# Optimization experiments

Hardware: AMD Instinct MI355X
Metric: run time of the kernel (lower is better)

Reference implementation:

```python
import jax, jax.numpy as jnp
import numpy as np

B, T, C, HS = 8, 2048, 1024, 64


def setup_inputs() -> dict:
    key = jax.random.key(0)
    ks = jax.random.split(key, 4)
    x = jax.random.normal(ks[0], (B, T, C), dtype=jnp.float32)
    Wq = jax.random.normal(ks[1], (C, HS), dtype=jnp.float32) * (C ** -0.5)
    Wk = jax.random.normal(ks[2], (C, HS), dtype=jnp.float32) * (C ** -0.5)
    Wv = jax.random.normal(ks[3], (C, HS), dtype=jnp.float32) * (C ** -0.5)
    mask = jnp.tril(jnp.ones((T, T), dtype=jnp.int32))  # causal mask
    return {"x": x, "mask": mask, "Wq": Wq, "Wk": Wk, "Wv": Wv}


def reference(x, mask, Wq, Wk, Wv):
    # x: [B,T,C]; bias-free projections to head_size
    q = jnp.einsum("btc,ch->bth", x, Wq)
    k = jnp.einsum("btc,ch->bth", x, Wk)
    v = jnp.einsum("btc,ch->bth", x, Wv)
    # NOTE: original scales by C**-0.5 (n_embd), not head_size**-0.5
    wei = jnp.einsum("bth,bsh->bts", q, k) * (x.shape[-1] ** -0.5)
    wei = jnp.where(mask[None, :, :] == 0, -jnp.inf, wei)
    wei = jax.nn.softmax(wei, axis=-1)
    # dropout is identity in eval / p=0
    out = jnp.einsum("bts,bsh->bth", wei, v)
    return out
```

## Files before the change

### kernel.cpp

```cpp
#include <hip/hip_runtime.h>
#include <hip/hip_bf16.h>


#define B_  8
#define T_  2048
#define C_  1024
#define HS_ 64
#define MROWS (B_ * T_)

typedef __attribute__((ext_vector_type(8))) short bf16x8;
typedef __attribute__((ext_vector_type(4))) float f32x4;
typedef __attribute__((ext_vector_type(4))) float float4v;

#define SCALE_LOG2 0.04508422037445829f

__device__ __forceinline__ short f2bs(float f) {
    __hip_bfloat16 h = __float2bfloat16(f);
    short s;
    __builtin_memcpy(&s, &h, 2);
    return s;
}

__global__ __launch_bounds__(256) void wt_kernel(
    const float* __restrict__ Wq,
    const float* __restrict__ Wk,
    const float* __restrict__ Wv,
    __hip_bfloat16* __restrict__ Wt) {
    __shared__ float tile[64][65];
    const int m  = blockIdx.x >> 4;
    const int r0 = (blockIdx.x & 15) * 64;
    const float* W = (m == 0) ? Wq : (m == 1) ? Wk : Wv;
    const int i = threadIdx.x >> 6;
    const int j = threadIdx.x & 63;
#pragma unroll
    for (int p = 0; p < 16; ++p) {
        int r = p * 4 + i;
        tile[r][j] = W[(size_t)(r0 + r) * HS_ + j];
    }
    __syncthreads();
#pragma unroll
    for (int p = 0; p < 16; ++p) {
        int h = p * 4 + i;
        Wt[(size_t)m * (HS_ * C_) + (size_t)h * C_ + r0 + j] =
            __float2bfloat16(tile[j][h]);
    }
}

__global__ __launch_bounds__(256, 2) void proj_kernel(
    const float* __restrict__ x,
    const __hip_bfloat16* __restrict__ Wt,
    __hip_bfloat16* __restrict__ Q,
    __hip_bfloat16* __restrict__ Kp,
    __hip_bfloat16* __restrict__ Vt)
{
    __shared__ float xt0[32 * 68];
    __shared__ float xt1[32 * 68];

    const int lane = threadIdx.x & 63;
    const int wave = threadIdx.x >> 6;
    const int quad = lane >> 4;
    const int l15  = lane & 15;
    const int row0 = blockIdx.x * 32;

    const float* gsrc[8];
#pragma unroll
    for (int rr = 0; rr < 8; ++rr)
        gsrc[rr] = x + (size_t)(row0 + wave * 8 + rr) * C_ + lane;

    const __hip_bfloat16* wbase[3];
#pragma unroll
    for (int j = 0; j < 3; ++j) {
        int nt = wave * 3 + j;
        int h  = ((nt & 3) * 16) + l15;
        wbase[j] = Wt + (size_t)(nt >> 2) * (HS_ * C_) + (size_t)h * C_ + quad * 8;
    }

    f32x4 acc[2][3];
#pragma unroll
    for (int rt = 0; rt < 2; ++rt)
#pragma unroll
        for (int j = 0; j < 3; ++j)
            acc[rt][j] = (f32x4){0.f, 0.f, 0.f, 0.f};

    bf16x8 bfr0[2][3], bfr1[2][3];

#define ISSUE_DMA(XT, kc)                                                    \
    do {                                                                     \
        _Pragma("unroll")                                                    \
        for (int rr = 0; rr < 8; ++rr)                                       \
            __builtin_amdgcn_global_load_lds(                                \
                (const __attribute__((address_space(1))) unsigned*)          \
                    (gsrc[rr] + (kc)),                                       \
                (__attribute__((address_space(3))) unsigned*)                \
                    (&XT[(wave * 8 + rr) * 68]),                             \
                4, 0, 0);                                                    \
    } while (0)

#define LOAD_B(BF, kc)                                                       \
    do {                                                                     \
        _Pragma("unroll")                                                    \
        for (int ks = 0; ks < 2; ++ks)                                       \
            _Pragma("unroll")                                                \
            for (int j = 0; j < 3; ++j)                                      \
                BF[ks][j] = *(const bf16x8*)(wbase[j] + (kc) + ks * 32);     \
    } while (0)

#define COMPUTE(XT, BF)                                                      \
    do {                                                                     \
        _Pragma("unroll")                                                    \
        for (int ks = 0; ks < 2; ++ks) {                                     \
            bf16x8 a[2];                                                     \
            _Pragma("unroll")                                                \
            for (int rt = 0; rt < 2; ++rt) {                                 \
                const float4v* p = (const float4v*)                          \
                    &XT[(rt * 16 + l15) * 68 + ks * 32 + quad * 8];          \
                float4v f0 = p[0], f1 = p[1];                                \
                _Pragma("unroll")                                            \
                for (int e = 0; e < 4; ++e) {                                \
                    a[rt][e]     = f2bs(f0[e]);                              \
                    a[rt][4 + e] = f2bs(f1[e]);                              \
                }                                                            \
            }                                                                \
            _Pragma("unroll")                                                \
            for (int rt = 0; rt < 2; ++rt)                                   \
                _Pragma("unroll")                                            \
                for (int j = 0; j < 3; ++j)                                  \
                    acc[rt][j] = __builtin_amdgcn_mfma_f32_16x16x32_bf16(    \
                        a[rt], BF[ks][j], acc[rt][j], 0, 0, 0);              \
        }                                                                    \
    } while (0)

    ISSUE_DMA(xt0, 0);
    LOAD_B(bfr0, 0);

#pragma unroll 1
    for (int kc = 0; kc < C_; kc += 128) {
        __syncthreads();
        if (kc + 64 < C_) {
            ISSUE_DMA(xt1, kc + 64);
            LOAD_B(bfr1, kc + 64);
        }
        COMPUTE(xt0, bfr0);
        __syncthreads();
        if (kc + 128 < C_) {
            ISSUE_DMA(xt0, kc + 128);
            LOAD_B(bfr0, kc + 128);
        }
        COMPUTE(xt1, bfr1);
    }
#undef ISSUE_DMA
#undef LOAD_B
#undef COMPUTE

#pragma unroll
    for (int rt = 0; rt < 2; ++rt) {
#pragma unroll
        for (int j = 0; j < 3; ++j) {
            int nt  = wave * 3 + j;
            int mtx = nt >> 2;
            int col = (nt & 3) * 16 + l15;
#pragma unroll
            for (int r = 0; r < 4; ++r) {
                int row = row0 + rt * 16 + quad * 4 + r;
                __hip_bfloat16 v = __float2bfloat16(acc[rt][j][r]);
                if (mtx == 0) {
                    Q[(size_t)row * HS_ + col] = v;
                } else if (mtx == 1) {
                    Kp[(size_t)row * HS_ + col] = v;
                } else {
                    int bidx = row >> 11;
                    int t    = row & 2047;
                    Vt[((size_t)bidx * HS_ + col) * T_ + t] = v;
                }
            }
        }
    }
}

__global__ __launch_bounds__(256, 3) void attn_kernel(
    const __hip_bfloat16* __restrict__ Q,
    const __hip_bfloat16* __restrict__ Kp,
    const __hip_bfloat16* __restrict__ Vt,
    float* __restrict__ out)
{
    __shared__ __align__(16) __hip_bfloat16 plds[4][16 * 64];
    __shared__ float o_lds[4][16][64];
    __shared__ float l_lds[4][16][16];

    const int tid  = threadIdx.x;
    const int wv   = tid >> 6;
    const int lane = tid & 63;
    const int quad = lane >> 4;
    const int l15  = lane & 15;
    const int b    = blockIdx.x & 7;
    const int lt   = 127 - (blockIdx.x >> 3);
    const int qb   = lt * 16;
    const int rowg = b * T_ + qb;

    bf16x8 qf0 = *(const bf16x8*)(Q + (size_t)(rowg + l15) * HS_ + quad * 8);
    bf16x8 qf1 = *(const bf16x8*)(Q + (size_t)(rowg + l15) * HS_ + 32 + quad * 8);

    f32x4 o[4];
#pragma unroll
    for (int j = 0; j < 4; ++j) o[j] = (f32x4){0.f, 0.f, 0.f, 0.f};
    float lp[4] = {0.f, 0.f, 0.f, 0.f};

    __hip_bfloat16* pb = plds[wv];
    const int nt = (qb + 15) / 64 + 1;

#pragma unroll 1
    for (int t = wv; t < nt; t += 4) {
        const int kb = t * 64;
        const __hip_bfloat16* Kb = Kp + (size_t)(b * T_ + kb) * HS_;

        bf16x8 kf[4][2];
#pragma unroll
        for (int c = 0; c < 4; ++c)
#pragma unroll
            for (int h = 0; h < 2; ++h)
                kf[c][h] = *(const bf16x8*)
                    (Kb + (size_t)(c * 16 + l15) * HS_ + h * 32 + quad * 8);
        bf16x8 vf[2][4];
#pragma unroll
        for (int h = 0; h < 2; ++h)
#pragma unroll
            for (int j = 0; j < 4; ++j)
                vf[h][j] = *(const bf16x8*)
                    (Vt + ((size_t)b * HS_ + j * 16 + l15) * T_ + kb + h * 32 + quad * 8);

        f32x4 s[4];
#pragma unroll
        for (int c = 0; c < 4; ++c) {
            s[c] = (f32x4){0.f, 0.f, 0.f, 0.f};
            s[c] = __builtin_amdgcn_mfma_f32_16x16x32_bf16(qf0, kf[c][0], s[c], 0, 0, 0);
            s[c] = __builtin_amdgcn_mfma_f32_16x16x32_bf16(qf1, kf[c][1], s[c], 0, 0, 0);
        }

        const bool msk = (kb + 63 > qb);
        float p[4][4];
#pragma unroll
        for (int c = 0; c < 4; ++c)
#pragma unroll
            for (int r = 0; r < 4; ++r) {
                p[c][r] = exp2f(s[c][r] * SCALE_LOG2);
                if (msk) {
                    int row = qb + quad * 4 + r;
                    if (kb + c * 16 + l15 > row) p[c][r] = 0.f;
                }
                lp[r] += p[c][r];
            }

#pragma unroll
        for (int r = 0; r < 4; ++r)
#pragma unroll
            for (int c = 0; c < 4; ++c)
                pb[(quad * 4 + r) * 64 + c * 16 + l15] = __float2bfloat16(p[c][r]);
        asm volatile("s_waitcnt lgkmcnt(0)" ::: "memory");
        bf16x8 pf0 = *(const bf16x8*)(pb + l15 * 64 + quad * 8);
        bf16x8 pf1 = *(const bf16x8*)(pb + l15 * 64 + 32 + quad * 8);

#pragma unroll
        for (int j = 0; j < 4; ++j) {
            o[j] = __builtin_amdgcn_mfma_f32_16x16x32_bf16(pf0, vf[0][j], o[j], 0, 0, 0);
            o[j] = __builtin_amdgcn_mfma_f32_16x16x32_bf16(pf1, vf[1][j], o[j], 0, 0, 0);
        }
    }

#pragma unroll
    for (int j = 0; j < 4; ++j)
#pragma unroll
        for (int r = 0; r < 4; ++r)
            o_lds[wv][quad * 4 + r][j * 16 + l15] = o[j][r];
#pragma unroll
    for (int r = 0; r < 4; ++r)
        l_lds[wv][quad * 4 + r][l15] = lp[r];
    __syncthreads();

    if (tid < 16) {
        float s = 0.f;
#pragma unroll
        for (int w = 0; w < 4; ++w)
            for (int c = 0; c < 16; ++c) s += l_lds[w][tid][c];
        l_lds[0][tid][0] = s;
    }
    __syncthreads();

    const int h = tid & 63;
#pragma unroll
    for (int k = 0; k < 4; ++k) {
        int row = (tid >> 6) * 4 + k;
        float s = o_lds[0][row][h] + o_lds[1][row][h] +
                  o_lds[2][row][h] + o_lds[3][row][h];
        out[(size_t)(rowg + row) * HS_ + h] = s / l_lds[0][row][0];
    }
}

extern "C" void kernel_launch(void* const* d_in, const int* in_sizes, int n_in,
                              void* d_out, int out_size, void* d_ws, size_t ws_size,
                              hipStream_t stream) {
    (void)in_sizes; (void)n_in; (void)out_size; (void)ws_size;
    const float* x  = (const float*)d_in[0];
    const float* Wq = (const float*)d_in[2];
    const float* Wk = (const float*)d_in[3];
    const float* Wv = (const float*)d_in[4];

    __hip_bfloat16* ws = (__hip_bfloat16*)d_ws;
    __hip_bfloat16* Wt = ws;
    __hip_bfloat16* Q  = ws + 196608;
    __hip_bfloat16* Kp = ws + 196608 + 1048576;
    __hip_bfloat16* Vt = ws + 196608 + 2 * 1048576;

    wt_kernel<<<48, 256, 0, stream>>>(Wq, Wk, Wv, Wt);
    proj_kernel<<<MROWS / 32, 256, 0, stream>>>(x, Wt, Q, Kp, Vt);
    attn_kernel<<<(T_ / 16) * B_, 256, 0, stream>>>(Q, Kp, Vt, (float*)d_out);
}
```

Measured before the change: 165.8 us.

## Double-buffer K/V register loads in attention loop and precompute reciprocal row sums

```diff
diff --git a/kernel.cpp b/kernel.cpp
--- a/kernel.cpp
+++ b/kernel.cpp
@@ -177,7 +177,7 @@
     }
 }
 
-__global__ __launch_bounds__(256, 3) void attn_kernel(
+__global__ __launch_bounds__(256, 2) void attn_kernel(
     const __hip_bfloat16* __restrict__ Q,
     const __hip_bfloat16* __restrict__ Kp,
     const __hip_bfloat16* __restrict__ Vt,
@@ -208,63 +208,79 @@
     __hip_bfloat16* pb = plds[wv];
     const int nt = (qb + 15) / 64 + 1;
 
+#define LOADKV(KF, VF, kb_)                                                  \
+    do {                                                                     \
+        const __hip_bfloat16* Kb_ = Kp + (size_t)(b * T_ + (kb_)) * HS_;     \
+        _Pragma("unroll")                                                    \
+        for (int c = 0; c < 4; ++c)                                          \
+            _Pragma("unroll")                                                \
+            for (int h = 0; h < 2; ++h)                                      \
+                KF[c][h] = *(const bf16x8*)                                  \
+                    (Kb_ + (size_t)(c * 16 + l15) * HS_ + h * 32 + quad * 8);\
+        _Pragma("unroll")                                                    \
+        for (int h = 0; h < 2; ++h)                                          \
+            _Pragma("unroll")                                                \
+            for (int j = 0; j < 4; ++j)                                      \
+                VF[h][j] = *(const bf16x8*)                                  \
+                    (Vt + ((size_t)b * HS_ + j * 16 + l15) * T_ +            \
+                     (kb_) + h * 32 + quad * 8);                             \
+    } while (0)
+
+#define PROC(KF, VF, kb_)                                                    \
+    do {                                                                     \
+        f32x4 s[4];                                                          \
+        _Pragma("unroll")                                                    \
+        for (int c = 0; c < 4; ++c) {                                        \
+            s[c] = (f32x4){0.f, 0.f, 0.f, 0.f};                              \
+            s[c] = __builtin_amdgcn_mfma_f32_16x16x32_bf16(                  \
+                qf0, KF[c][0], s[c], 0, 0, 0);                               \
+            s[c] = __builtin_amdgcn_mfma_f32_16x16x32_bf16(                  \
+                qf1, KF[c][1], s[c], 0, 0, 0);                               \
+        }                                                                    \
+        const bool msk = ((kb_) + 63 > qb);                                  \
+        float p[4][4];                                                       \
+        _Pragma("unroll")                                                    \
+        for (int c = 0; c < 4; ++c)                                          \
+            _Pragma("unroll")                                                \
+            for (int r = 0; r < 4; ++r) {                                    \
+                p[c][r] = exp2f(s[c][r] * SCALE_LOG2);                       \
+                if (msk) {                                                   \
+                    int row = qb + quad * 4 + r;                             \
+                    if ((kb_) + c * 16 + l15 > row) p[c][r] = 0.f;           \
+                }                                                            \
+                lp[r] += p[c][r];                                            \
+            }                                                                \
+        _Pragma("unroll")                                                    \
+        for (int r = 0; r < 4; ++r)                                          \
+            _Pragma("unroll")                                                \
+            for (int c = 0; c < 4; ++c)                                      \
+                pb[(quad * 4 + r) * 64 + c * 16 + l15] =                     \
+                    __float2bfloat16(p[c][r]);                               \
+        asm volatile("s_waitcnt lgkmcnt(0)" ::: "memory");                   \
+        bf16x8 pf0 = *(const bf16x8*)(pb + l15 * 64 + quad * 8);             \
+        bf16x8 pf1 = *(const bf16x8*)(pb + l15 * 64 + 32 + quad * 8);        \
+        _Pragma("unroll")                                                    \
+        for (int j = 0; j < 4; ++j) {                                        \
+            o[j] = __builtin_amdgcn_mfma_f32_16x16x32_bf16(                  \
+                pf0, VF[0][j], o[j], 0, 0, 0);                               \
+            o[j] = __builtin_amdgcn_mfma_f32_16x16x32_bf16(                  \
+                pf1, VF[1][j], o[j], 0, 0, 0);                               \
+        }                                                                    \
+    } while (0)
+
+    bf16x8 kA[4][2], vA[2][4], kB[4][2], vB[2][4];
+    if (wv < nt) LOADKV(kA, vA, wv * 64);
+    int i = 0;
 #pragma unroll 1
-    for (int t = wv; t < nt; t += 4) {
-        const int kb = t * 64;
-        const __hip_bfloat16* Kb = Kp + (size_t)(b * T_ + kb) * HS_;
-
-        bf16x8 kf[4][2];
-#pragma unroll
-        for (int c = 0; c < 4; ++c)
-#pragma unroll
-            for (int h = 0; h < 2; ++h)
-                kf[c][h] = *(const bf16x8*)
-                    (Kb + (size_t)(c * 16 + l15) * HS_ + h * 32 + quad * 8);
-        bf16x8 vf[2][4];
-#pragma unroll
-        for (int h = 0; h < 2; ++h)
-#pragma unroll
-            for (int j = 0; j < 4; ++j)
-                vf[h][j] = *(const bf16x8*)
-                    (Vt + ((size_t)b * HS_ + j * 16 + l15) * T_ + kb + h * 32 + quad * 8);
-
-        f32x4 s[4];
-#pragma unroll
-        for (int c = 0; c < 4; ++c) {
-            s[c] = (f32x4){0.f, 0.f, 0.f, 0.f};
-            s[c] = __builtin_amdgcn_mfma_f32_16x16x32_bf16(qf0, kf[c][0], s[c], 0, 0, 0);
-            s[c] = __builtin_amdgcn_mfma_f32_16x16x32_bf16(qf1, kf[c][1], s[c], 0, 0, 0);
-        }
-
-        const bool msk = (kb + 63 > qb);
-        float p[4][4];
-#pragma unroll
-        for (int c = 0; c < 4; ++c)
-#pragma unroll
-            for (int r = 0; r < 4; ++r) {
-                p[c][r] = exp2f(s[c][r] * SCALE_LOG2);
-                if (msk) {
-                    int row = qb + quad * 4 + r;
-                    if (kb + c * 16 + l15 > row) p[c][r] = 0.f;
-                }
-                lp[r] += p[c][r];
-            }
-
-#pragma unroll
-        for (int r = 0; r < 4; ++r)
-#pragma unroll
-            for (int c = 0; c < 4; ++c)
-                pb[(quad * 4 + r) * 64 + c * 16 + l15] = __float2bfloat16(p[c][r]);
-        asm volatile("s_waitcnt lgkmcnt(0)" ::: "memory");
-        bf16x8 pf0 = *(const bf16x8*)(pb + l15 * 64 + quad * 8);
-        bf16x8 pf1 = *(const bf16x8*)(pb + l15 * 64 + 32 + quad * 8);
-
-#pragma unroll
-        for (int j = 0; j < 4; ++j) {
-            o[j] = __builtin_amdgcn_mfma_f32_16x16x32_bf16(pf0, vf[0][j], o[j], 0, 0, 0);
-            o[j] = __builtin_amdgcn_mfma_f32_16x16x32_bf16(pf1, vf[1][j], o[j], 0, 0, 0);
-        }
-    }
+    for (; wv + 4 * (i + 1) < nt; i += 2) {
+        LOADKV(kB, vB, (wv + 4 * (i + 1)) * 64);
+        PROC(kA, vA, (wv + 4 * i) * 64);
+        if (wv + 4 * (i + 2) < nt) LOADKV(kA, vA, (wv + 4 * (i + 2)) * 64);
+        PROC(kB, vB, (wv + 4 * (i + 1)) * 64);
+    }
+    if (wv + 4 * i < nt) PROC(kA, vA, (wv + 4 * i) * 64);
+#undef LOADKV
+#undef PROC
 
 #pragma unroll
     for (int j = 0; j < 4; ++j)
@@ -281,7 +297,7 @@
 #pragma unroll
         for (int w = 0; w < 4; ++w)
             for (int c = 0; c < 16; ++c) s += l_lds[w][tid][c];
-        l_lds[0][tid][0] = s;
+        l_lds[0][tid][0] = 1.0f / s;
     }
     __syncthreads();
 
@@ -291,7 +307,7 @@
         int row = (tid >> 6) * 4 + k;
         float s = o_lds[0][row][h] + o_lds[1][row][h] +
                   o_lds[2][row][h] + o_lds[3][row][h];
-        out[(size_t)(rowg + row) * HS_ + h] = s / l_lds[0][row][0];
+        out[(size_t)(rowg + row) * HS_ + h] = s * l_lds[0][row][0];
     }
 }
 
```

New measurement: 163.2 us. No clear change (-1.6%).

## Process 32 query rows per attention block to reuse K/V tiles, pad P in LDS

Applied to the files above, without the earlier changes.

```diff
diff --git a/kernel.cpp b/kernel.cpp
--- a/kernel.cpp
+++ b/kernel.cpp
@@ -13,6 +13,8 @@
 typedef __attribute__((ext_vector_type(4))) float float4v;
 
 #define SCALE_LOG2 0.04508422037445829f
+
+#define PSTR 72
 
 __device__ __forceinline__ short f2bs(float f) {
     __hip_bfloat16 h = __float2bfloat16(f);
@@ -46,7 +48,7 @@
     }
 }
 
-__global__ __launch_bounds__(256, 2) void proj_kernel(
+__global__ __launch_bounds__(256, 4) void proj_kernel(
     const float* __restrict__ x,
     const __hip_bfloat16* __restrict__ Wt,
     __hip_bfloat16* __restrict__ Q,
@@ -183,9 +185,10 @@
     const __hip_bfloat16* __restrict__ Vt,
     float* __restrict__ out)
 {
-    __shared__ __align__(16) __hip_bfloat16 plds[4][16 * 64];
-    __shared__ float o_lds[4][16][64];
-    __shared__ float l_lds[4][16][16];
+    __shared__ __align__(16) char smem[4 * 32 * PSTR * 2 + 4 * 32 * 4];
+    __hip_bfloat16* plds = (__hip_bfloat16*)smem;
+    float* o_red = (float*)smem;
+    float* l_red = (float*)(smem + 4 * 32 * PSTR * 2);
 
     const int tid  = threadIdx.x;
     const int wv   = tid >> 6;
@@ -193,20 +196,28 @@
     const int quad = lane >> 4;
     const int l15  = lane & 15;
     const int b    = blockIdx.x & 7;
-    const int lt   = 127 - (blockIdx.x >> 3);
-    const int qb   = lt * 16;
+    const int lt   = 63 - (blockIdx.x >> 3);
+    const int qb   = lt * 32;
     const int rowg = b * T_ + qb;
 
-    bf16x8 qf0 = *(const bf16x8*)(Q + (size_t)(rowg + l15) * HS_ + quad * 8);
-    bf16x8 qf1 = *(const bf16x8*)(Q + (size_t)(rowg + l15) * HS_ + 32 + quad * 8);
-
-    f32x4 o[4];
-#pragma unroll
-    for (int j = 0; j < 4; ++j) o[j] = (f32x4){0.f, 0.f, 0.f, 0.f};
-    float lp[4] = {0.f, 0.f, 0.f, 0.f};
-
-    __hip_bfloat16* pb = plds[wv];
-    const int nt = (qb + 15) / 64 + 1;
+    __hip_bfloat16* pb = plds + wv * (32 * PSTR);
+
+    bf16x8 qf[2][2];
+#pragma unroll
+    for (int rt = 0; rt < 2; ++rt)
+#pragma unroll
+        for (int h = 0; h < 2; ++h)
+            qf[rt][h] = *(const bf16x8*)
+                (Q + (size_t)(rowg + rt * 16 + l15) * HS_ + h * 32 + quad * 8);
+
+    f32x4 o[2][4];
+#pragma unroll
+    for (int rt = 0; rt < 2; ++rt)
+#pragma unroll
+        for (int j = 0; j < 4; ++j) o[rt][j] = (f32x4){0.f, 0.f, 0.f, 0.f};
+    float lp[2][4] = {{0.f,0.f,0.f,0.f},{0.f,0.f,0.f,0.f}};
+
+    const int nt = (qb + 31) / 64 + 1;
 
 #pragma unroll 1
     for (int t = wv; t < nt; t += 4) {
@@ -226,72 +237,101 @@
 #pragma unroll
             for (int j = 0; j < 4; ++j)
                 vf[h][j] = *(const bf16x8*)
-                    (Vt + ((size_t)b * HS_ + j * 16 + l15) * T_ + kb + h * 32 + quad * 8);
-
-        f32x4 s[4];
-#pragma unroll
-        for (int c = 0; c < 4; ++c) {
-            s[c] = (f32x4){0.f, 0.f, 0.f, 0.f};
-            s[c] = __builtin_amdgcn_mfma_f32_16x16x32_bf16(qf0, kf[c][0], s[c], 0, 0, 0);
-            s[c] = __builtin_amdgcn_mfma_f32_16x16x32_bf16(qf1, kf[c][1], s[c], 0, 0, 0);
-        }
+                    (Vt + ((size_t)b * HS_ + j * 16 + l15) * T_ +
+                     kb + h * 32 + quad * 8);
+
+        f32x4 s[2][4];
+#pragma unroll
+        for (int rt = 0; rt < 2; ++rt)
+#pragma unroll
+            for (int c = 0; c < 4; ++c) {
+                s[rt][c] = (f32x4){0.f, 0.f, 0.f, 0.f};
+                s[rt][c] = __builtin_amdgcn_mfma_f32_16x16x32_bf16(
+                    qf[rt][0], kf[c][0], s[rt][c], 0, 0, 0);
+                s[rt][c] = __builtin_amdgcn_mfma_f32_16x16x32_bf16(
+                    qf[rt][1], kf[c][1], s[rt][c], 0, 0, 0);
+            }
 
         const bool msk = (kb + 63 > qb);
-        float p[4][4];
-#pragma unroll
-        for (int c = 0; c < 4; ++c)
-#pragma unroll
-            for (int r = 0; r < 4; ++r) {
-                p[c][r] = exp2f(s[c][r] * SCALE_LOG2);
-                if (msk) {
-                    int row = qb + quad * 4 + r;
-                    if (kb + c * 16 + l15 > row) p[c][r] = 0.f;
+#pragma unroll
+        for (int rt = 0; rt < 2; ++rt)
+#pragma unroll
+            for (int c = 0; c < 4; ++c)
+#pragma unroll
+                for (int r = 0; r < 4; ++r) {
+                    float pv = exp2f(s[rt][c][r] * SCALE_LOG2);
+                    if (msk) {
+                        int row = qb + rt * 16 + quad * 4 + r;
+                        if (kb + c * 16 + l15 > row) pv = 0.f;
+                    }
+                    lp[rt][r] += pv;
+                    pb[(rt * 16 + quad * 4 + r) * PSTR + c * 16 + l15] =
+                        __float2bfloat16(pv);
                 }
-                lp[r] += p[c][r];
+        asm volatile("s_waitcnt lgkmcnt(0)" ::: "memory");
+#pragma unroll
+        for (int rt = 0; rt < 2; ++rt) {
+            bf16x8 pf0 = *(const bf16x8*)
+                (pb + (rt * 16 + l15) * PSTR + quad * 8);
+            bf16x8 pf1 = *(const bf16x8*)
+                (pb + (rt * 16 + l15) * PSTR + 32 + quad * 8);
+#pragma unroll
+            for (int j = 0; j < 4; ++j) {
+                o[rt][j] = __builtin_amdgcn_mfma_f32_16x16x32_bf16(
+                    pf0, vf[0][j], o[rt][j], 0, 0, 0);
+                o[rt][j] = __builtin_amdgcn_mfma_f32_16x16x32_bf16(
+                    pf1, vf[1][j], o[rt][j], 0, 0, 0);
             }
-
+        }
+    }
+
+#pragma unroll
+    for (int rt = 0; rt < 2; ++rt)
+#pragma unroll
+        for (int r = 0; r < 4; ++r) {
+            float v = lp[rt][r];
+            v += __shfl_xor(v, 1);
+            v += __shfl_xor(v, 2);
+            v += __shfl_xor(v, 4);
+            v += __shfl_xor(v, 8);
+            if (l15 == 0)
+                l_red[wv * 32 + rt * 16 + quad * 4 + r] = v;
+        }
+    __syncthreads();
+
+    const int h  = tid & 63;
+    const int rg = tid >> 6;
+
+#pragma unroll
+    for (int j = 0; j < 4; ++j)
 #pragma unroll
         for (int r = 0; r < 4; ++r)
-#pragma unroll
-            for (int c = 0; c < 4; ++c)
-                pb[(quad * 4 + r) * 64 + c * 16 + l15] = __float2bfloat16(p[c][r]);
-        asm volatile("s_waitcnt lgkmcnt(0)" ::: "memory");
-        bf16x8 pf0 = *(const bf16x8*)(pb + l15 * 64 + quad * 8);
-        bf16x8 pf1 = *(const bf16x8*)(pb + l15 * 64 + 32 + quad * 8);
-
-#pragma unroll
-        for (int j = 0; j < 4; ++j) {
-            o[j] = __builtin_amdgcn_mfma_f32_16x16x32_bf16(pf0, vf[0][j], o[j], 0, 0, 0);
-            o[j] = __builtin_amdgcn_mfma_f32_16x16x32_bf16(pf1, vf[1][j], o[j], 0, 0, 0);
-        }
-    }
+            o_red[(wv * 16 + quad * 4 + r) * 64 + j * 16 + l15] = o[0][j][r];
+    __syncthreads();
+#pragma unroll
+    for (int k = 0; k < 4; ++k) {
+        int row = rg * 4 + k;
+        float s = o_red[(0 * 16 + row) * 64 + h] + o_red[(1 * 16 + row) * 64 + h]
+                + o_red[(2 * 16 + row) * 64 + h] + o_red[(3 * 16 + row) * 64 + h];
+        float l = l_red[row] + l_red[32 + row] + l_red[64 + row] + l_red[96 + row];
+        out[(size_t)(rowg + row) * HS_ + h] = s / l;
+    }
+    __syncthreads();
 
 #pragma unroll
     for (int j = 0; j < 4; ++j)
 #pragma unroll
         for (int r = 0; r < 4; ++r)
-            o_lds[wv][quad * 4 + r][j * 16 + l15] = o[j][r];
-#pragma unroll
-    for (int r = 0; r < 4; ++r)
-        l_lds[wv][quad * 4 + r][l15] = lp[r];
-    __syncthreads();
-
-    if (tid < 16) {
-        float s = 0.f;
-#pragma unroll
-        for (int w = 0; w < 4; ++w)
-            for (int c = 0; c < 16; ++c) s += l_lds[w][tid][c];
-        l_lds[0][tid][0] = s;
-    }
-    __syncthreads();
-
-    const int h = tid & 63;
+            o_red[(wv * 16 + quad * 4 + r) * 64 + j * 16 + l15] = o[1][j][r];
+    __syncthreads();
 #pragma unroll
     for (int k = 0; k < 4; ++k) {
-        int row = (tid >> 6) * 4 + k;
-        float s = o_lds[0][row][h] + o_lds[1][row][h] +
-                  o_lds[2][row][h] + o_lds[3][row][h];
-        out[(size_t)(rowg + row) * HS_ + h] = s / l_lds[0][row][0];
+        int row16 = rg * 4 + k;
+        int row   = 16 + row16;
+        float s = o_red[(0 * 16 + row16) * 64 + h] + o_red[(1 * 16 + row16) * 64 + h]
+                + o_red[(2 * 16 + row16) * 64 + h] + o_red[(3 * 16 + row16) * 64 + h];
+        float l = l_red[row] + l_red[32 + row] + l_red[64 + row] + l_red[96 + row];
+        out[(size_t)(rowg + row) * HS_ + h] = s / l;
     }
 }
 
@@ -312,5 +352,5 @@
 
     wt_kernel<<<48, 256, 0, stream>>>(Wq, Wk, Wv, Wt);
     proj_kernel<<<MROWS / 32, 256, 0, stream>>>(x, Wt, Q, Kp, Vt);
-    attn_kernel<<<(T_ / 16) * B_, 256, 0, stream>>>(Q, Kp, Vt, (float*)d_out);
-}
+    attn_kernel<<<(T_ / 32) * B_, 256, 0, stream>>>(Q, Kp, Vt, (float*)d_out);
+}
```

After: 156.0 us. 1.06x faster.
